# Optimization experiments

Hardware: AMD Instinct MI355X
Metric: run time of the kernel (lower is better)

## Reference

```python
import jax, jax.numpy as jnp
import numpy as np

S, SM, B, D, H, NHEAD = 1024, 1024, 4, 1024, 2048, 16
EPS = 1e-5


def layer_norm(x, g, b):
    mu = jnp.mean(x, axis=-1, keepdims=True)
    var = jnp.var(x, axis=-1, keepdims=True)
    return (x - mu) * jax.lax.rsqrt(var + EPS) * g + b


def mha(q_in, k_in, v_in, w_in, b_in, w_out, b_out):
    # q_in: [Sq,B,D], k_in/v_in: [Sk,B,D]; torch nn.MultiheadAttention math (eval)
    Sq, Bn, Dn = q_in.shape
    Sk = k_in.shape[0]
    hd = Dn // NHEAD
    wq, wk, wv = jnp.split(w_in, 3, axis=0)
    bq, bk, bv = jnp.split(b_in, 3)
    q = (q_in @ wq.T + bq) * (hd ** -0.5)
    k = k_in @ wk.T + bk
    v = v_in @ wv.T + bv
    rs = lambda x, L: x.reshape(L, Bn, NHEAD, hd).transpose(1, 2, 0, 3)  # [B,h,L,hd]
    qh, kh, vh = rs(q, Sq), rs(k, Sk), rs(v, Sk)
    att = jax.nn.softmax(jnp.einsum('bhqd,bhkd->bhqk', qh, kh), axis=-1)
    o = jnp.einsum('bhqk,bhkd->bhqd', att, vh).transpose(2, 0, 1, 3).reshape(Sq, Bn, Dn)
    return o @ w_out.T + b_out


def sru(x, w, v, b):
    # SRU cell with input projection (n_in != n_out -> k=4): candidate, f, r, highway
    Ssz, Bsz, _ = x.shape
    U = (x @ w).reshape(Ssz, Bsz, 4, H)  # [S,B,4,H]
    vf, vr = v[0], v[1]
    bf, br = b[0], b[1]

    def step(c, u):
        xc, fp, rp, xh = u[:, 0], u[:, 1], u[:, 2], u[:, 3]
        f = jax.nn.sigmoid(fp + vf * c + bf)
        r = jax.nn.sigmoid(rp + vr * c + br)
        c2 = f * c + (1.0 - f) * xc
        h = r * c2 + (1.0 - r) * xh
        return c2, h

    c0 = jnp.zeros((Bsz, H), x.dtype)
    _, hs = jax.lax.scan(step, c0, U)
    return hs  # [S,B,H]


def setup_inputs():
    key = jax.random.key(0)
    ks = jax.random.split(key, 12)
    n = lambda k, shp, sc=0.02: jax.random.normal(k, shp, dtype=jnp.float32) * sc
    return dict(
        tgt=n(ks[0], (S, B, D), 1.0),
        memory=n(ks[1], (SM, B, D), 1.0),
        sa_w_in=n(ks[2], (3 * D, D)), sa_b_in=jnp.zeros((3 * D,)),
        sa_w_out=n(ks[3], (D, D)), sa_b_out=jnp.zeros((D,)),
        ca_w_in=n(ks[4], (3 * D, D)), ca_b_in=jnp.zeros((3 * D,)),
        ca_w_out=n(ks[5], (D, D)), ca_b_out=jnp.zeros((D,)),
        sru_w=n(ks[6], (D, 4 * H)), sru_v=n(ks[7], (2, H)), sru_b=jnp.zeros((2, H)),
        lin2_w=n(ks[8], (D, H)), lin2_b=jnp.zeros((D,)),
        ln1_g=jnp.ones((D,)), ln1_b=jnp.zeros((D,)),
        ln2_g=jnp.ones((D,)), ln2_b=jnp.zeros((D,)),
        ln3_g=jnp.ones((D,)), ln3_b=jnp.zeros((D,)),
    )


def reference(tgt, memory, sa_w_in, sa_b_in, sa_w_out, sa_b_out,
              ca_w_in, ca_b_in, ca_w_out, ca_b_out,
              sru_w, sru_v, sru_b, lin2_w, lin2_b,
              ln1_g, ln1_b, ln2_g, ln2_b, ln3_g, ln3_b):
    # dropout layers are identity in eval mode
    t2 = mha(tgt, tgt, tgt, sa_w_in, sa_b_in, sa_w_out, sa_b_out)
    t = layer_norm(tgt + t2, ln1_g, ln1_b)
    t2 = mha(t, memory, memory, ca_w_in, ca_b_in, ca_w_out, ca_b_out)
    t = layer_norm(t + t2, ln2_g, ln2_b)
    h = sru(t, sru_w, sru_v, sru_b)
    t2 = h @ lin2_w.T + lin2_b
    t = layer_norm(t + t2, ln3_g, ln3_b)
    return t
```

## Files before the change

kernel.cpp:

```cpp
#include <hip/hip_runtime.h>
#include <hip/hip_bf16.h>

typedef __bf16 bf16;
typedef bf16 bf16x8 __attribute__((ext_vector_type(8)));
typedef bf16 bf16x4 __attribute__((ext_vector_type(4)));
typedef float f32x4 __attribute__((ext_vector_type(4)));

#define MFMA16(a, b, c) __builtin_amdgcn_mfma_f32_16x16x32_bf16((a), (b), (c), 0, 0, 0)

__device__ __forceinline__ void gl_lds16(const void* g, void* l) {
    __builtin_amdgcn_global_load_lds((const __attribute__((address_space(1))) void*)g,
                                     (__attribute__((address_space(3))) void*)l, 16, 0, 0);
}

__global__ __launch_bounds__(256) void k_detect(const void* __restrict__ src, int* __restrict__ flag) {
    __shared__ int cnt;
    if (threadIdx.x == 0) cnt = 0;
    __syncthreads();
    const unsigned int* w = (const unsigned int*)src;
    int local = 0;
    for (int i = threadIdx.x; i < 4096; i += 256) {
        unsigned int e = (w[i] >> 7) & 0xFF;
        local += (e > 100 && e < 150) ? 1 : 0;
    }
    atomicAdd(&cnt, local);
    __syncthreads();
    if (threadIdx.x == 0) *flag = (cnt > 2048) ? 1 : 0;
}

struct BigSegs {
    const void* src[6];
    bf16* dst[6];
    int cum[7];
};
__global__ __launch_bounds__(256) void k_norm_big(const int* __restrict__ flag, BigSegs s) {
    int seg = 0;
#pragma unroll
    for (int t = 0; t < 5; t++) seg += (blockIdx.x >= s.cum[t + 1]) ? 1 : 0;
    int i = (blockIdx.x - s.cum[seg]) * 256 + threadIdx.x;
    const void* sp = s.src[seg];
    bf16* dp = s.dst[seg];
    if (*flag) {
        ((bf16x8*)dp)[i] = ((const bf16x8*)sp)[i];
    } else {
        const float* fs = (const float*)sp + (size_t)i * 8;
        bf16x8 o;
#pragma unroll
        for (int j = 0; j < 8; j++) o[j] = (bf16)fs[j];
        ((bf16x8*)dp)[i] = o;
    }
}

struct SmallSegs {
    const void* src[13];
    bf16* dst[13];
    int n8[13];
};
__global__ __launch_bounds__(256) void k_norm_multi(const int* __restrict__ flag, SmallSegs s) {
    int seg = blockIdx.x;
    const void* sp = s.src[seg];
    bf16* dp = s.dst[seg];
    int n = s.n8[seg];
    int f = *flag;
    for (int i = threadIdx.x; i < n; i += 256) {
        if (f) {
            ((bf16x8*)dp)[i] = ((const bf16x8*)sp)[i];
        } else {
            const float* fs = (const float*)sp + (size_t)i * 8;
            bf16x8 o;
#pragma unroll
            for (int j = 0; j < 8; j++) o[j] = (bf16)fs[j];
            ((bf16x8*)dp)[i] = o;
        }
    }
}

__global__ __launch_bounds__(256) void k_cvt(const int* __restrict__ flag, const void* __restrict__ in,
                                             float* __restrict__ out, bf16* __restrict__ outb) {
    size_t i = (size_t)blockIdx.x * 256 + threadIdx.x;
    f32x4 a, b;
    bf16x8 v;
    if (*flag) {
        v = ((const bf16x8*)in)[i];
#pragma unroll
        for (int j = 0; j < 4; j++) { a[j] = (float)v[j]; b[j] = (float)v[4 + j]; }
    } else {
        a = ((const f32x4*)in)[i * 2];
        b = ((const f32x4*)in)[i * 2 + 1];
#pragma unroll
        for (int j = 0; j < 4; j++) { v[j] = (bf16)a[j]; v[4 + j] = (bf16)b[j]; }
    }
    ((f32x4*)out)[i * 2] = a;
    ((f32x4*)out)[i * 2 + 1] = b;
    ((bf16x8*)outb)[i] = v;
}

__global__ __launch_bounds__(256) void k_transpose(const int* __restrict__ flag, const void* __restrict__ in,
                                                   bf16* __restrict__ out, int R, int C) {
    __shared__ __align__(16) bf16 t[64][72];
    int tid = threadIdx.x;
    int c0 = blockIdx.x * 64, r0 = blockIdx.y * 64;
#pragma unroll
    for (int i = 0; i < 2; i++) {
        int idx = tid + i * 256;
        int r = idx >> 3, ch = idx & 7;
        size_t base = (size_t)(r0 + r) * C + c0 + ch * 8;
        bf16x8 v;
        if (*flag) {
            v = *(const bf16x8*)((const bf16*)in + base);
        } else {
            const float* f = (const float*)in + base;
            f32x4 x = *(const f32x4*)f, y = *(const f32x4*)(f + 4);
#pragma unroll
            for (int j = 0; j < 4; j++) { v[j] = (bf16)x[j]; v[4 + j] = (bf16)y[j]; }
        }
        *(bf16x8*)&t[r][ch * 8] = v;
    }
    __syncthreads();
    int nbase = c0 & 2047, joff = c0 >> 11;
#pragma unroll
    for (int i = 0; i < 2; i++) {
        int idx = tid + i * 256;
        int cr = idx >> 3, ch = idx & 7;
        bf16x8 v;
#pragma unroll
        for (int j = 0; j < 8; j++) v[j] = t[ch * 8 + j][cr];
        int np = (nbase + cr) * 4 + joff;
        *(bf16x8*)(out + (size_t)np * R + r0 + ch * 8) = v;
    }
}

__global__ __launch_bounds__(256) void k_vtr(const bf16* __restrict__ in, int ldv, bf16* __restrict__ out) {
    int nt = blockIdx.x, st = blockIdx.y, b = blockIdx.z;
    __shared__ __align__(16) bf16 t[64][72];
    int tid = threadIdx.x;
#pragma unroll
    for (int i = 0; i < 2; i++) {
        int idx = tid + i * 256;
        int r = idx >> 3, ch = idx & 7;
        bf16x8 v = *(const bf16x8*)(in + (size_t)((st * 64 + r) * 4 + b) * ldv + nt * 64 + ch * 8);
        *(bf16x8*)&t[r][ch * 8] = v;
    }
    __syncthreads();
#pragma unroll
    for (int i = 0; i < 2; i++) {
        int idx = tid + i * 256;
        int dr = idx >> 3, ch = idx & 7;
        bf16x8 v;
#pragma unroll
        for (int j = 0; j < 8; j++) v[j] = t[ch * 8 + j][dr];
        *(bf16x8*)(out + (size_t)(b * 1024 + nt * 64 + dr) * 1024 + st * 64 + ch * 8) = v;
    }
}

__device__ __forceinline__ int swzB(int r, int byteInRow) {
    return r * 128 + (byteInRow ^ ((r & 7) << 4));
}

template <int BM>
__global__ __launch_bounds__(256) void k_gemm(
    const bf16* __restrict__ A, int lda,
    const bf16* __restrict__ W, int ldw,
    const bf16* __restrict__ bias,
    float* __restrict__ Cf, bf16* __restrict__ Cb, int ldc,
    int K, int scale_end, float scale) {
    constexpr int MI = BM / 32;
    __shared__ __align__(16) char Asm[BM * 128];
    __shared__ __align__(16) char Bsm[128 * 128];
    int tid = threadIdx.x, w = tid >> 6, l = tid & 63, lg = l >> 4, lm = l & 15;
    int wm = w >> 1, wn = w & 1;
    int m0 = blockIdx.y * BM, n0 = blockIdx.x * 128;

    f32x4 acc[MI][4] = {};

    for (int k0 = 0; k0 < K; k0 += 64) {
#pragma unroll
        for (int i = 0; i < BM / 32; i++) {
            int r = i * 32 + w * 8 + (l >> 3);
            int gs = (l & 7) ^ (r & 7);
            gl_lds16(A + (size_t)(m0 + r) * lda + k0 + gs * 8,
                     Asm + (i * 32 + w * 8) * 128);
        }
#pragma unroll
        for (int i = 0; i < 4; i++) {
            int r = i * 32 + w * 8 + (l >> 3);
            int gs = (l & 7) ^ (r & 7);
            gl_lds16(W + (size_t)(n0 + r) * ldw + k0 + gs * 8,
                     Bsm + (i * 32 + w * 8) * 128);
        }
        __syncthreads();
#pragma unroll
        for (int kh = 0; kh < 2; kh++) {
            bf16x8 af[MI], bfr[4];
#pragma unroll
            for (int i = 0; i < MI; i++)
                af[i] = *(const bf16x8*)(Asm + swzB(wm * (BM / 2) + i * 16 + lm, kh * 64 + lg * 16));
#pragma unroll
            for (int j = 0; j < 4; j++)
                bfr[j] = *(const bf16x8*)(Bsm + swzB(wn * 64 + j * 16 + lm, kh * 64 + lg * 16));
#pragma unroll
            for (int i = 0; i < MI; i++)
#pragma unroll
                for (int j = 0; j < 4; j++)
                    acc[i][j] = MFMA16(af[i], bfr[j], acc[i][j]);
        }
        __syncthreads();
    }
#pragma unroll
    for (int j = 0; j < 4; j++) {
        int col = n0 + wn * 64 + j * 16 + lm;
        float bv = bias ? (float)bias[col] : 0.f;
        float sc = (col < scale_end) ? scale : 1.f;
#pragma unroll
        for (int i = 0; i < MI; i++) {
            int row = m0 + wm * (BM / 2) + i * 16 + lg * 4;
#pragma unroll
            for (int r = 0; r < 4; r++) {
                float v = (acc[i][j][r] + bv) * sc;
                size_t idx = (size_t)(row + r) * ldc + col;
                if (Cf) Cf[idx] = v;
                if (Cb) Cb[idx] = (bf16)v;
            }
        }
    }
}

__device__ __forceinline__ int swz2(int row, int byteInRow) {
    return row * 128 + (byteInRow ^ ((row & 7) << 4));
}
__device__ __forceinline__ int swzP(int row, int byteInRow) {
    return row * 128 + (byteInRow ^ ((row & 3) << 4) ^ (((row >> 2) & 1) << 6));
}

__global__ __launch_bounds__(256) void k_attn(
    const bf16* __restrict__ Qp, const bf16* __restrict__ Kp, const bf16* __restrict__ Vt,
    int ldq, int ldk, bf16* __restrict__ Op) {
    int h = blockIdx.x & 15, b = blockIdx.x >> 4, qblk = blockIdx.y;
    int tid = threadIdx.x, w = tid >> 6, l = tid & 63, lg = l >> 4, lm = l & 15;
    int r0 = tid >> 3, ch = tid & 7;

    __shared__ __align__(16) char Ksm[64 * 128];
    __shared__ __align__(16) char Vsm[64 * 128];
    __shared__ __align__(16) char Psm[4][32 * 128];

    bf16x8 qf[2][2];
#pragma unroll
    for (int u = 0; u < 2; u++) {
        int qrow = qblk * 128 + w * 32 + u * 16 + lm;
#pragma unroll
        for (int kk = 0; kk < 2; kk++)
            qf[u][kk] = *(const bf16x8*)(Qp + (size_t)(qrow * 4 + b) * ldq + h * 64 + kk * 32 + lg * 8);
    }

    const bf16* vbase = Vt + (size_t)(b * 1024 + h * 64) * 1024;

    bf16x8 kreg[2], vreg[2];
#pragma unroll
    for (int p = 0; p < 2; p++) {
        int r = r0 + p * 32;
        kreg[p] = *(const bf16x8*)(Kp + (size_t)(r * 4 + b) * ldk + h * 64 + ch * 8);
        vreg[p] = *(const bf16x8*)(vbase + (size_t)r * 1024 + ch * 8);
    }

    f32x4 oa[2][4] = {};
    float mrun[2][4], lrun[2][4];
#pragma unroll
    for (int u = 0; u < 2; u++)
#pragma unroll
        for (int r = 0; r < 4; r++) { mrun[u][r] = -1e30f; lrun[u][r] = 0.f; }

    for (int kt = 0; kt < 16; kt++) {
        __syncthreads();
#pragma unroll
        for (int p = 0; p < 2; p++) {
            int r = r0 + p * 32;
            *(bf16x8*)(Ksm + swz2(r, ch * 16)) = kreg[p];
            *(bf16x8*)(Vsm + swz2(r, ch * 16)) = vreg[p];
        }
        if (kt < 15) {
#pragma unroll
            for (int p = 0; p < 2; p++) {
                int r = (kt + 1) * 64 + r0 + p * 32;
                kreg[p] = *(const bf16x8*)(Kp + (size_t)(r * 4 + b) * ldk + h * 64 + ch * 8);
                vreg[p] = *(const bf16x8*)(vbase + (size_t)(r0 + p * 32) * 1024 + (kt + 1) * 64 + ch * 8);
            }
        }
        __syncthreads();

        f32x4 sc[2][4] = {};
#pragma unroll
        for (int kk = 0; kk < 2; kk++)
#pragma unroll
            for (int jt = 0; jt < 4; jt++) {
                bf16x8 bk = *(const bf16x8*)(Ksm + swz2(jt * 16 + lm, kk * 64 + lg * 16));
#pragma unroll
                for (int u = 0; u < 2; u++)
                    sc[u][jt] = MFMA16(qf[u][kk], bk, sc[u][jt]);
            }

        float m_[2][4];
#pragma unroll
        for (int u = 0; u < 2; u++)
#pragma unroll
            for (int r = 0; r < 4; r++) {
                float m = fmaxf(fmaxf(sc[u][0][r], sc[u][1][r]), fmaxf(sc[u][2][r], sc[u][3][r]));
#pragma unroll
                for (int d = 1; d < 16; d <<= 1) m = fmaxf(m, __shfl_xor(m, d));
                m_[u][r] = m;
            }
        bool grow = false;
#pragma unroll
        for (int u = 0; u < 2; u++)
#pragma unroll
            for (int r = 0; r < 4; r++) grow = grow || (m_[u][r] > mrun[u][r] + 8.f);
        if (__any(grow)) {
#pragma unroll
            for (int u = 0; u < 2; u++)
#pragma unroll
                for (int r = 0; r < 4; r++) {
                    float mn = fmaxf(mrun[u][r], m_[u][r]);
                    float al = __expf(mrun[u][r] - mn);
                    mrun[u][r] = mn;
                    lrun[u][r] *= al;
#pragma unroll
                    for (int ot = 0; ot < 4; ot++) oa[u][ot][r] *= al;
                }
        }
#pragma unroll
        for (int u = 0; u < 2; u++)
#pragma unroll
            for (int jt = 0; jt < 4; jt++)
#pragma unroll
                for (int r = 0; r < 4; r++) {
                    float p = __expf(sc[u][jt][r] - mrun[u][r]);
                    sc[u][jt][r] = p;
                    lrun[u][r] += p;
                }
#pragma unroll
        for (int u = 0; u < 2; u++)
#pragma unroll
            for (int jt = 0; jt < 4; jt++)
#pragma unroll
                for (int r = 0; r < 4; r++)
                    *(bf16*)(Psm[w] + swzP(u * 16 + lg * 4 + r, (jt * 16 + lm) * 2)) = (bf16)sc[u][jt][r];
        asm volatile("s_waitcnt lgkmcnt(0)" ::: "memory");
        __builtin_amdgcn_sched_barrier(0);
#pragma unroll
        for (int kk = 0; kk < 2; kk++) {
            bf16x8 pa[2];
#pragma unroll
            for (int u = 0; u < 2; u++)
                pa[u] = *(const bf16x8*)(Psm[w] + swzP(u * 16 + lm, kk * 64 + lg * 16));
#pragma unroll
            for (int ot = 0; ot < 4; ot++) {
                bf16x8 bv = *(const bf16x8*)(Vsm + swz2(ot * 16 + lm, kk * 64 + lg * 16));
#pragma unroll
                for (int u = 0; u < 2; u++)
                    oa[u][ot] = MFMA16(pa[u], bv, oa[u][ot]);
            }
        }
    }
#pragma unroll
    for (int u = 0; u < 2; u++)
#pragma unroll
        for (int r = 0; r < 4; r++) {
#pragma unroll
            for (int d = 1; d < 16; d <<= 1) lrun[u][r] += __shfl_xor(lrun[u][r], d);
            float inv = 1.f / lrun[u][r];
            int srow = qblk * 128 + w * 32 + u * 16 + lg * 4 + r;
#pragma unroll
            for (int ot = 0; ot < 4; ot++) {
                int col = h * 64 + ot * 16 + lm;
                Op[(size_t)(srow * 4 + b) * 1024 + col] = (bf16)(oa[u][ot][r] * inv);
            }
        }
}

template <typename XT>
__global__ __launch_bounds__(256) void k_addln(
    const XT* __restrict__ X, const float* __restrict__ Yd,
    const bf16* __restrict__ g, const bf16* __restrict__ bb,
    float* __restrict__ outF, bf16* __restrict__ outB) {
    int row = blockIdx.x * 4 + (threadIdx.x >> 6);
    int l = threadIdx.x & 63;
    const XT* xr = X + (size_t)row * 1024;
    const float* yr = Yd + (size_t)row * 1024;
    float v[16];
    float s = 0.f, s2 = 0.f;
#pragma unroll
    for (int q = 0; q < 4; q++) {
        float xa[4];
        if constexpr (sizeof(XT) == 4) {
            f32x4 a = *(const f32x4*)(xr + l * 4 + q * 256);
#pragma unroll
            for (int j = 0; j < 4; j++) xa[j] = a[j];
        } else {
            bf16x4 a = *(const bf16x4*)(xr + l * 4 + q * 256);
#pragma unroll
            for (int j = 0; j < 4; j++) xa[j] = (float)a[j];
        }
        f32x4 c = *(const f32x4*)(yr + l * 4 + q * 256);
#pragma unroll
        for (int j = 0; j < 4; j++) {
            float t = xa[j] + c[j];
            v[q * 4 + j] = t;
            s += t;
            s2 += t * t;
        }
    }
#pragma unroll
    for (int d = 1; d < 64; d <<= 1) { s += __shfl_xor(s, d); s2 += __shfl_xor(s2, d); }
    float mu = s * (1.f / 1024.f);
    float var = s2 * (1.f / 1024.f) - mu * mu;
    float rstd = rsqrtf(var + 1e-5f);
#pragma unroll
    for (int q = 0; q < 4; q++)
#pragma unroll
        for (int j = 0; j < 4; j++) {
            int col = l * 4 + q * 256 + j;
            float y = (v[q * 4 + j] - mu) * rstd * (float)g[col] + (float)bb[col];
            if (outF) outF[(size_t)row * 1024 + col] = y;
            if (outB) outB[(size_t)row * 1024 + col] = (bf16)y;
        }
}

__global__ __launch_bounds__(64) void k_sru(
    const bf16* __restrict__ U, const bf16* __restrict__ v2, const bf16* __restrict__ b2,
    bf16* __restrict__ Hb) {
    int ch = blockIdx.x * 64 + threadIdx.x;
    int b = ch >> 11, hh = ch & 2047;
    float vf = (float)v2[hh], vr = (float)v2[2048 + hh];
    float bfv = (float)b2[hh], brv = (float)b2[2048 + hh];
    float c = 0.f;
    const bf16x4* u = (const bf16x4*)(U + (size_t)b * 8192 + (size_t)hh * 4);
    bf16* ho = Hb + (size_t)b * 2048 + hh;
    bf16x4 q[8];
#pragma unroll
    for (int i = 0; i < 8; i++) q[i] = u[(size_t)i * 8192];
    for (int it = 0; it < 128; it++) {
#pragma unroll
        for (int j = 0; j < 8; j++) {
            int ls = it * 8 + j;
            bf16x4 v = q[j];
            if (ls + 8 < 1024) q[j] = u[(size_t)(ls + 8) * 8192];
            float xc = (float)v[0], fp = (float)v[1], rp = (float)v[2], xh = (float)v[3];
            float f = 1.f / (1.f + __expf(-(fp + vf * c + bfv)));
            float r = 1.f / (1.f + __expf(-(rp + vr * c + brv)));
            c = f * c + (1.f - f) * xc;
            float hv = r * c + (1.f - r) * xh;
            ho[(size_t)ls * 8192] = (bf16)hv;
        }
    }
}

extern "C" void kernel_launch(void* const* d_in, const int* in_sizes, int n_in,
                              void* d_out, int out_size, void* d_ws, size_t ws_size,
                              hipStream_t stream) {
    const size_t MB = 1u << 20;
    char* ws = (char*)d_ws;

    bf16* memB    = (bf16*)(ws + 0);
    bf16* sawinB  = (bf16*)(ws + 8 * MB);
    bf16* sawoutB = (bf16*)(ws + 14 * MB);
    bf16* cawinB  = (bf16*)(ws + 16 * MB);
    bf16* cawoutB = (bf16*)(ws + 22 * MB);
    bf16* lin2wB  = (bf16*)(ws + 24 * MB);
    char* S0 = ws + 28 * MB;
    bf16* sabinB  = (bf16*)(S0 + 0 * 8192);
    bf16* cabinB  = (bf16*)(S0 + 1 * 8192);
    bf16* saboutB = (bf16*)(S0 + 2 * 8192);
    bf16* caboutB = (bf16*)(S0 + 3 * 8192);
    bf16* lin2bB  = (bf16*)(S0 + 4 * 8192);
    bf16* sruvB   = (bf16*)(S0 + 5 * 8192);
    bf16* srubB   = (bf16*)(S0 + 6 * 8192);
    bf16* ln1gB   = (bf16*)(S0 + 7 * 8192);
    bf16* ln1bB   = (bf16*)(S0 + 8 * 8192);
    bf16* ln2gB   = (bf16*)(S0 + 9 * 8192);
    bf16* ln2bB   = (bf16*)(S0 + 10 * 8192);
    bf16* ln3gB   = (bf16*)(S0 + 11 * 8192);
    bf16* ln3bB   = (bf16*)(S0 + 12 * 8192);
    int*  flag    = (int*)(S0 + 13 * 8192);

    char* P = ws + 29 * MB;
    float* t0   = (float*)(P + 0);
    bf16*  qkv  = (bf16*)(P + 16 * MB);
    bf16*  qca  = qkv;
    bf16*  kvca = (bf16*)(P + 24 * MB);
    bf16*  obuf = (bf16*)(P + 40 * MB);
    bf16*  Vt   = (bf16*)(P + 56 * MB);
    bf16*  t0b  = (bf16*)(P + 64 * MB);
    float* tmp  = (float*)(P + 64 * MB);
    bf16*  t1   = (bf16*)(P + 80 * MB);
    bf16*  t2   = (bf16*)(ws + 0);
    bf16*  wT   = (bf16*)(P + 0);
    bf16*  U    = (bf16*)(P + 16 * MB);
    bf16*  hb   = (bf16*)(P + 80 * MB);
    float* tmp2 = (float*)(P + 16 * MB);

    k_detect<<<1, 256, 0, stream>>>(d_in[0], flag);
    BigSegs bg;
    {
        const void* bsrc[6] = {d_in[1], d_in[2], d_in[4], d_in[6], d_in[8], d_in[13]};
        bf16* bdst[6] = {memB, sawinB, sawoutB, cawinB, cawoutB, lin2wB};
        const int cum[7] = {0, 2048, 3584, 4096, 5632, 6144, 7168};
        for (int i = 0; i < 6; i++) { bg.src[i] = bsrc[i]; bg.dst[i] = bdst[i]; }
        for (int i = 0; i < 7; i++) bg.cum[i] = cum[i];
    }
    k_norm_big<<<7168, 256, 0, stream>>>(flag, bg);
    SmallSegs sg;
    const int srcIdx[13] = {3, 7, 5, 9, 14, 11, 12, 15, 16, 17, 18, 19, 20};
    bf16* dsts[13] = {sabinB, cabinB, saboutB, caboutB, lin2bB, sruvB, srubB,
                      ln1gB, ln1bB, ln2gB, ln2bB, ln3gB, ln3bB};
    const int n8s[13] = {384, 384, 128, 128, 128, 512, 512, 128, 128, 128, 128, 128, 128};
    for (int i = 0; i < 13; i++) { sg.src[i] = d_in[srcIdx[i]]; sg.dst[i] = dsts[i]; sg.n8[i] = n8s[i]; }
    k_norm_multi<<<13, 256, 0, stream>>>(flag, sg);

    k_cvt<<<2048, 256, 0, stream>>>(flag, d_in[0], t0, t0b);

    k_gemm<128><<<dim3(24, 32), 256, 0, stream>>>(t0b, 1024, sawinB, 1024, sabinB,
                                                  nullptr, qkv, 3072, 1024, 1024, 0.125f);
    k_vtr<<<dim3(16, 16, 4), 256, 0, stream>>>(qkv + 2048, 3072, Vt);
    k_attn<<<dim3(64, 8), 256, 0, stream>>>(qkv, qkv + 1024, Vt, 3072, 3072, obuf);
    k_gemm<64><<<dim3(8, 64), 256, 0, stream>>>(obuf, 1024, sawoutB, 1024, saboutB,
                                                tmp, nullptr, 1024, 1024, 0, 1.f);
    k_addln<float><<<1024, 256, 0, stream>>>(t0, tmp, ln1gB, ln1bB, nullptr, t1);

    k_gemm<64><<<dim3(8, 64), 256, 0, stream>>>(t1, 1024, cawinB, 1024, cabinB,
                                                nullptr, qca, 1024, 1024, 1024, 0.125f);
    k_gemm<128><<<dim3(16, 32), 256, 0, stream>>>(memB, 1024, cawinB + (size_t)1024 * 1024, 1024,
                                                  cabinB + 1024, nullptr, kvca, 2048, 1024, 0, 1.f);
    k_vtr<<<dim3(16, 16, 4), 256, 0, stream>>>(kvca + 1024, 2048, Vt);
    k_attn<<<dim3(64, 8), 256, 0, stream>>>(qca, kvca, Vt, 1024, 2048, obuf);
    k_gemm<64><<<dim3(8, 64), 256, 0, stream>>>(obuf, 1024, cawoutB, 1024, caboutB,
                                                tmp, nullptr, 1024, 1024, 0, 1.f);
    k_addln<bf16><<<1024, 256, 0, stream>>>(t1, tmp, ln2gB, ln2bB, nullptr, t2);

    k_transpose<<<dim3(128, 16), 256, 0, stream>>>(flag, d_in[10], wT, 1024, 8192);
    k_gemm<128><<<dim3(64, 32), 256, 0, stream>>>(t2, 1024, wT, 1024,
                                                  nullptr, nullptr, U, 8192, 1024, 0, 1.f);
    k_sru<<<128, 64, 0, stream>>>(U, sruvB, srubB, hb);
    k_gemm<64><<<dim3(8, 64), 256, 0, stream>>>(hb, 2048, lin2wB, 2048, lin2bB,
                                                tmp2, nullptr, 1024, 2048, 0, 1.f);
    k_addln<bf16><<<1024, 256, 0, stream>>>(t2, tmp2, ln3gB, ln3bB, (float*)d_out, nullptr);
}
```

Baseline: 552.3 us.

## Scatter SRU projection output into per-channel contiguous layout for sequential scan

The GEMM producing the SRU input projection now writes its output in a channel-major layout, so each (batch, hidden) channel's 1024 timesteps × 4 gates sit contiguously. The SRU scan kernel then reads 16-byte vectors covering two timesteps from a contiguous stream instead of 8-byte strided loads 16 KB apart. This is meant to cut the latency of the serial scan's memory reads, at the cost of scattered 2-byte stores in the GEMM epilogue.

```diff
diff --git a/kernel.cpp b/kernel.cpp
--- a/kernel.cpp
+++ b/kernel.cpp
@@ -157,7 +157,7 @@
     return r * 128 + (byteInRow ^ ((r & 7) << 4));
 }
 
-template <int BM>
+template <int BM, bool USCAT>
 __global__ __launch_bounds__(256) void k_gemm(
     const bf16* __restrict__ A, int lda,
     const bf16* __restrict__ W, int ldw,
@@ -217,9 +217,16 @@
 #pragma unroll
             for (int r = 0; r < 4; r++) {
                 float v = (acc[i][j][r] + bv) * sc;
-                size_t idx = (size_t)(row + r) * ldc + col;
-                if (Cf) Cf[idx] = v;
-                if (Cb) Cb[idx] = (bf16)v;
+                if constexpr (USCAT) {
+                    int rw = row + r;
+                    int ch = (rw & 3) * 2048 + (col >> 2);
+                    size_t idx = (size_t)ch * 4096 + (size_t)(rw >> 2) * 4 + (col & 3);
+                    Cb[idx] = (bf16)v;
+                } else {
+                    size_t idx = (size_t)(row + r) * ldc + col;
+                    if (Cf) Cf[idx] = v;
+                    if (Cb) Cb[idx] = (bf16)v;
+                }
             }
         }
     }
@@ -425,30 +432,34 @@
 }
 
 __global__ __launch_bounds__(64) void k_sru(
-    const bf16* __restrict__ U, const bf16* __restrict__ v2, const bf16* __restrict__ b2,
+    const bf16* __restrict__ U2, const bf16* __restrict__ v2, const bf16* __restrict__ b2,
     bf16* __restrict__ Hb) {
     int ch = blockIdx.x * 64 + threadIdx.x;
     int b = ch >> 11, hh = ch & 2047;
     float vf = (float)v2[hh], vr = (float)v2[2048 + hh];
     float bfv = (float)b2[hh], brv = (float)b2[2048 + hh];
     float c = 0.f;
-    const bf16x4* u = (const bf16x4*)(U + (size_t)b * 8192 + (size_t)hh * 4);
+    const bf16x8* u = (const bf16x8*)(U2 + (size_t)ch * 4096);
     bf16* ho = Hb + (size_t)b * 2048 + hh;
-    bf16x4 q[8];
-#pragma unroll
-    for (int i = 0; i < 8; i++) q[i] = u[(size_t)i * 8192];
-    for (int it = 0; it < 128; it++) {
-#pragma unroll
-        for (int j = 0; j < 8; j++) {
-            int ls = it * 8 + j;
-            bf16x4 v = q[j];
-            if (ls + 8 < 1024) q[j] = u[(size_t)(ls + 8) * 8192];
-            float xc = (float)v[0], fp = (float)v[1], rp = (float)v[2], xh = (float)v[3];
-            float f = 1.f / (1.f + __expf(-(fp + vf * c + bfv)));
-            float r = 1.f / (1.f + __expf(-(rp + vr * c + brv)));
-            c = f * c + (1.f - f) * xc;
-            float hv = r * c + (1.f - r) * xh;
-            ho[(size_t)ls * 8192] = (bf16)hv;
+    bf16x8 q[16];
+#pragma unroll
+    for (int i = 0; i < 16; i++) q[i] = u[i];
+    for (int it = 0; it < 32; it++) {
+#pragma unroll
+        for (int j = 0; j < 16; j++) {
+            int cidx = it * 16 + j;
+            bf16x8 v = q[j];
+            if (cidx + 16 < 512) q[j] = u[cidx + 16];
+#pragma unroll
+            for (int t = 0; t < 2; t++) {
+                float xc = (float)v[t * 4 + 0], fp = (float)v[t * 4 + 1];
+                float rp = (float)v[t * 4 + 2], xh = (float)v[t * 4 + 3];
+                float f = 1.f / (1.f + __expf(-(fp + vf * c + bfv)));
+                float r = 1.f / (1.f + __expf(-(rp + vr * c + brv)));
+                c = f * c + (1.f - f) * xc;
+                float hv = r * c + (1.f - r) * xh;
+                ho[(size_t)(cidx * 2 + t) * 8192] = (bf16)hv;
+            }
         }
     }
 }
@@ -493,7 +504,7 @@
     bf16*  t1   = (bf16*)(P + 80 * MB);
     bf16*  t2   = (bf16*)(ws + 0);
     bf16*  wT   = (bf16*)(P + 0);
-    bf16*  U    = (bf16*)(P + 16 * MB);
+    bf16*  U2   = (bf16*)(P + 16 * MB);
     bf16*  hb   = (bf16*)(P + 80 * MB);
     float* tmp2 = (float*)(P + 16 * MB);
 
@@ -517,29 +528,29 @@
 
     k_cvt<<<2048, 256, 0, stream>>>(flag, d_in[0], t0, t0b);
 
-    k_gemm<128><<<dim3(24, 32), 256, 0, stream>>>(t0b, 1024, sawinB, 1024, sabinB,
-                                                  nullptr, qkv, 3072, 1024, 1024, 0.125f);
+    k_gemm<128, false><<<dim3(24, 32), 256, 0, stream>>>(t0b, 1024, sawinB, 1024, sabinB,
+                                                         nullptr, qkv, 3072, 1024, 1024, 0.125f);
     k_vtr<<<dim3(16, 16, 4), 256, 0, stream>>>(qkv + 2048, 3072, Vt);
     k_attn<<<dim3(64, 8), 256, 0, stream>>>(qkv, qkv + 1024, Vt, 3072, 3072, obuf);
-    k_gemm<64><<<dim3(8, 64), 256, 0, stream>>>(obuf, 1024, sawoutB, 1024, saboutB,
-                                                tmp, nullptr, 1024, 1024, 0, 1.f);
+    k_gemm<64, false><<<dim3(8, 64), 256, 0, stream>>>(obuf, 1024, sawoutB, 1024, saboutB,
+                                                       tmp, nullptr, 1024, 1024, 0, 1.f);
     k_addln<float><<<1024, 256, 0, stream>>>(t0, tmp, ln1gB, ln1bB, nullptr, t1);
 
-    k_gemm<64><<<dim3(8, 64), 256, 0, stream>>>(t1, 1024, cawinB, 1024, cabinB,
-                                                nullptr, qca, 1024, 1024, 1024, 0.125f);
-    k_gemm<128><<<dim3(16, 32), 256, 0, stream>>>(memB, 1024, cawinB + (size_t)1024 * 1024, 1024,
-                                                  cabinB + 1024, nullptr, kvca, 2048, 1024, 0, 1.f);
+    k_gemm<64, false><<<dim3(8, 64), 256, 0, stream>>>(t1, 1024, cawinB, 1024, cabinB,
+                                                       nullptr, qca, 1024, 1024, 1024, 0.125f);
+    k_gemm<128, false><<<dim3(16, 32), 256, 0, stream>>>(memB, 1024, cawinB + (size_t)1024 * 1024, 1024,
+                                                         cabinB + 1024, nullptr, kvca, 2048, 1024, 0, 1.f);
     k_vtr<<<dim3(16, 16, 4), 256, 0, stream>>>(kvca + 1024, 2048, Vt);
     k_attn<<<dim3(64, 8), 256, 0, stream>>>(qca, kvca, Vt, 1024, 2048, obuf);
-    k_gemm<64><<<dim3(8, 64), 256, 0, stream>>>(obuf, 1024, cawoutB, 1024, caboutB,
-                                                tmp, nullptr, 1024, 1024, 0, 1.f);
+    k_gemm<64, false><<<dim3(8, 64), 256, 0, stream>>>(obuf, 1024, cawoutB, 1024, caboutB,
+                                                       tmp, nullptr, 1024, 1024, 0, 1.f);
     k_addln<bf16><<<1024, 256, 0, stream>>>(t1, tmp, ln2gB, ln2bB, nullptr, t2);
 
     k_transpose<<<dim3(128, 16), 256, 0, stream>>>(flag, d_in[10], wT, 1024, 8192);
-    k_gemm<128><<<dim3(64, 32), 256, 0, stream>>>(t2, 1024, wT, 1024,
-                                                  nullptr, nullptr, U, 8192, 1024, 0, 1.f);
-    k_sru<<<128, 64, 0, stream>>>(U, sruvB, srubB, hb);
-    k_gemm<64><<<dim3(8, 64), 256, 0, stream>>>(hb, 2048, lin2wB, 2048, lin2bB,
-                                                tmp2, nullptr, 1024, 2048, 0, 1.f);
+    k_gemm<128, true><<<dim3(64, 32), 256, 0, stream>>>(t2, 1024, wT, 1024,
+                                                        nullptr, nullptr, U2, 0, 1024, 0, 1.f);
+    k_sru<<<128, 64, 0, stream>>>(U2, sruvB, srubB, hb);
+    k_gemm<64, false><<<dim3(8, 64), 256, 0, stream>>>(hb, 2048, lin2wB, 2048, lin2bB,
+                                                       tmp2, nullptr, 1024, 2048, 0, 1.f);
     k_addln<bf16><<<1024, 256, 0, stream>>>(t2, tmp2, ln3gB, ln3bB, (float*)d_out, nullptr);
 }
```

Result: faster. 518.5 us (-6.1%).
